# Kernel optimization log

Measured on AMD Instinct MI355X. Metric: run time of the kernel, lower is better.

Reference implementation:

```python
import jax, jax.numpy as jnp
import numpy as np

N, T, D, H1, H2, NH = 4096, 2048, 256, 128, 32, 4
ALPHA = 0.2  # LeakyReLU slope in GAT
NEG = -9e15  # mask value for non-edges


def _gat(x, adj, W, a_src, a_dst, fc_W, fc_b):
    # Multi-head GAT (pygat style), heads stacked on leading axis, then Linear fc.
    Wh = jnp.einsum('nd,hde->hne', x, W)                    # [NH, n, d_out]
    f = jnp.einsum('hne,he->hn', Wh, a_src)                 # a^T [Wh_i || .]
    g = jnp.einsum('hne,he->hn', Wh, a_dst)                 # a^T [. || Wh_j]
    e = jax.nn.leaky_relu(f[:, :, None] + g[:, None, :], ALPHA)  # [NH, n, n]
    e = jnp.where(adj[None, :, :] > 0, e, NEG)
    att = jax.nn.softmax(e, axis=-1)
    h = jax.nn.elu(jnp.einsum('hnm,hme->hne', att, Wh))     # concat=True -> ELU
    h = jnp.transpose(h, (1, 0, 2)).reshape(x.shape[0], -1)  # [n, NH*d_out]
    return h @ fc_W + fc_b


def setup_inputs() -> dict:
    key = jax.random.key(0)
    ks = jax.random.split(key, 24)
    s = 0.1
    x = jax.random.normal(ks[0], (N, D), jnp.float32)
    t_x = jax.random.normal(ks[1], (T, D), jnp.float32)
    adj = (jax.random.uniform(ks[2], (N, N)) < 0.005).astype(jnp.float32) + jnp.eye(N, dtype=jnp.float32)
    t_adj = (jax.random.uniform(ks[3], (T, T)) < 0.01).astype(jnp.float32) + jnp.eye(T, dtype=jnp.float32)
    tfidf_x = jax.random.uniform(ks[4], (T, N), jnp.float32) * 0.01
    p = lambda k, shp: jax.random.normal(k, shp, jnp.float32) * s
    return {
        'x': x, 'adj': adj, 't_x': t_x, 't_adj': t_adj, 'tfidf_x': tfidf_x,
        # concept-graph MHGAT (in D -> per-head D, concat NH*D -> fc -> D)
        'gat_W': p(ks[5], (NH, D, D)), 'gat_asrc': p(ks[6], (NH, D)), 'gat_adst': p(ks[7], (NH, D)),
        'gat_fcW': p(ks[8], (NH * D, D)), 'gat_fcb': jnp.zeros((D,), jnp.float32),
        # text-graph MHGAT
        't_W': p(ks[9], (NH, D, D)), 't_asrc': p(ks[10], (NH, D)), 't_adst': p(ks[11], (NH, D)),
        't_fcW': p(ks[12], (NH * D, D)), 't_fcb': jnp.zeros((D,), jnp.float32),
        # gated fusion fc
        'fus_W': p(ks[13], (D, D)), 'fus_b': jnp.zeros((D,), jnp.float32),
        # GCN encoder weights (Kipf VGAE GraphConvolution: adj @ (x @ W))
        'gc1_W': p(ks[14], (D, H1)), 'gc2_W': p(ks[15], (H1, H2)), 'gc3_W': p(ks[16], (H1, H2)),
    }


def reference(x, adj, t_x, t_adj, tfidf_x,
              gat_W, gat_asrc, gat_adst, gat_fcW, gat_fcb,
              t_W, t_asrc, t_adst, t_fcW, t_fcb,
              fus_W, fus_b, gc1_W, gc2_W, gc3_W):
    # gated fusion of concept-graph and text-graph GAT outputs (eval mode, dropout off)
    concept = _gat(x, adj, gat_W, gat_asrc, gat_adst, gat_fcW, gat_fcb)      # [N, D]
    gat_text = _gat(t_x, t_adj, t_W, t_asrc, t_adst, t_fcW, t_fcb)           # [T, D]
    c_text = tfidf_x.T @ gat_text                                            # [N, D]
    z = jax.nn.sigmoid(concept + c_text)
    fusion = (z * concept + (1.0 - z) * c_text) @ fus_W + fus_b              # [N, D]
    # GCN VAE encoder
    h1 = jax.nn.relu(adj @ (fusion @ gc1_W))                                 # [N, H1]
    mu = adj @ (h1 @ gc2_W)                                                  # [N, H2]
    logvar = adj @ (h1 @ gc3_W)                                              # [N, H2]
    # eval-mode reparameterize -> z_lat = mu; decoder act is identity in GCNModelVAE
    recon = mu @ mu.T                                                        # [N, N]
    return recon, mu, logvar
```

## Files before the change

kernel.cpp:

```cpp
#include <hip/hip_runtime.h>
#include <hip/hip_bf16.h>

#define MAX_E 128
typedef __attribute__((ext_vector_type(8))) short bf16x8;
typedef __attribute__((ext_vector_type(4))) float f32x4;

__device__ __forceinline__ unsigned short f2bf(float f) {
    union { float f; unsigned u; } a; a.f = f;
    unsigned r = a.u + 0x7FFFu + ((a.u >> 16) & 1u);
    return (unsigned short)(r >> 16);
}
__device__ __forceinline__ float bf2f(unsigned short s) {
    union { unsigned u; float f; } a; a.u = ((unsigned)s) << 16; return a.f;
}
__device__ __forceinline__ float wave_sum(float v) {
#pragma unroll
    for (int o = 1; o < 64; o <<= 1) v += __shfl_xor(v, o, 64);
    return v;
}
__device__ __forceinline__ float wave_max(float v) {
#pragma unroll
    for (int o = 1; o < 64; o <<= 1) v = fmaxf(v, __shfl_xor(v, o, 64));
    return v;
}

#define MAXJ 16
struct TJobs {
    const float* src[MAXJ];
    unsigned short* dst[MAXJ];
    int R[MAXJ], C[MAXJ], tb[MAXJ];
    int njobs;
};

__global__ __launch_bounds__(256) void prep_k(
        const float* __restrict__ adj, const float* __restrict__ t_adj,
        int* __restrict__ cnt, int* __restrict__ eidx_c, int* __restrict__ eidx_t,
        const float* __restrict__ gat_W, const float* __restrict__ gat_asrc,
        const float* __restrict__ gat_adst, const float* __restrict__ t_W,
        const float* __restrict__ t_asrc, const float* __restrict__ t_adst,
        float* __restrict__ APDP,
        const float* __restrict__ fus_W, const float* __restrict__ fus_b,
        const float* __restrict__ gc1_W, unsigned short* __restrict__ W2T,
        float* __restrict__ B2,
        const float* __restrict__ x, const float* __restrict__ t_x,
        unsigned short* __restrict__ XBF, unsigned short* __restrict__ TXBF,
        int w2_base, int cast_base, TJobs tj) {
    __shared__ float smem[2080];
    int bid = blockIdx.x, tid = threadIdx.x;
    if (bid < 6144) {
        int* s_cnt = (int*)smem;
        if (tid == 0) *s_cnt = 0;
        __syncthreads();
        if (bid < 4096) {
            const float4* ar = (const float4*)(adj + (size_t)bid * 4096);
            int* er = eidx_c + (size_t)bid * MAX_E;
            float4 v0 = ar[tid], v1 = ar[tid + 256], v2 = ar[tid + 512], v3 = ar[tid + 768];
            float va[16] = {v0.x, v0.y, v0.z, v0.w, v1.x, v1.y, v1.z, v1.w,
                            v2.x, v2.y, v2.z, v2.w, v3.x, v3.y, v3.z, v3.w};
#pragma unroll
            for (int it = 0; it < 4; it++) {
                int jb = (tid + it * 256) * 4;
#pragma unroll
                for (int c = 0; c < 4; c++) {
                    float vv = va[it * 4 + c];
                    if (vv > 0.f) {
                        int p = atomicAdd(s_cnt, 1);
                        if (p < MAX_E) er[p] = (jb + c) | (vv > 1.5f ? 0x40000000 : 0);
                    }
                }
            }
        } else {
            int r = bid - 4096;
            const float4* ar = (const float4*)(t_adj + (size_t)r * 2048);
            int* er = eidx_t + (size_t)r * MAX_E;
            float4 v0 = ar[tid], v1 = ar[tid + 256];
            float va[8] = {v0.x, v0.y, v0.z, v0.w, v1.x, v1.y, v1.z, v1.w};
#pragma unroll
            for (int it = 0; it < 2; it++) {
                int jb = (tid + it * 256) * 4;
#pragma unroll
                for (int c = 0; c < 4; c++) {
                    if (va[it * 4 + c] > 0.f) {
                        int p = atomicAdd(s_cnt, 1);
                        if (p < MAX_E) er[p] = jb + c;
                    }
                }
            }
        }
        __syncthreads();
        if (tid == 0) cnt[bid] = *s_cnt < MAX_E ? *s_cnt : MAX_E;
    } else if (bid < 6152) {
        int pb = bid - 6144, h = pb & 3, g = pb >> 2, d = tid;
        const float* W  = g ? t_W : gat_W;
        const float* as = g ? t_asrc : gat_asrc;
        const float* ad = g ? t_adst : gat_adst;
        float* sa = smem; float* sd = smem + 256;
        sa[d] = as[h * 256 + d]; sd[d] = ad[h * 256 + d];
        __syncthreads();
        const float* wr = W + (size_t)h * 65536 + (size_t)d * 256;
        float ap = 0.f, dp = 0.f;
        for (int e = 0; e < 256; e++) { float w = wr[e]; ap += w * sa[e]; dp += w * sd[e]; }
        APDP[g * 1024 + h * 256 + d] = ap;
        APDP[2048 + g * 1024 + h * 256 + d] = dp;
    } else if (bid < w2_base) {
        int local = bid - 6152;
        int j = 0;
        while (j + 1 < tj.njobs && local >= tj.tb[j + 1]) j++;
        local -= tj.tb[j];
        int R = tj.R[j], C = tj.C[j];
        int xt = C >> 5;
        int tx = local % xt, ty = local / xt;
        const float* in = tj.src[j];
        unsigned short* outp = tj.dst[j];
        float (*t)[33] = (float(*)[33])smem;
        int jj = tid & 31, ii = tid >> 5;
        int r0 = ty * 32, c0 = tx * 32;
#pragma unroll
        for (int k = 0; k < 4; k++) { int rl = ii + k * 8; t[rl][jj] = in[(size_t)(r0 + rl) * C + c0 + jj]; }
        __syncthreads();
#pragma unroll
        for (int k = 0; k < 4; k++) { int cl = ii + k * 8; outp[(size_t)(c0 + cl) * R + r0 + jj] = f2bf(t[jj][cl]); }
    } else if (bid < w2_base + 32) {
        int bW = bid - w2_base;
        int n0 = (bW & 3) * 32, k0 = (bW >> 2) * 32;
        int nn = tid & 31, kb = (tid >> 5) * 4;
        float (*s_a)[65] = (float(*)[65])smem;
        float acc[4] = {0.f, 0.f, 0.f, 0.f};
        for (int ec = 0; ec < 4; ec++) {
            for (int t = tid; t < 32 * 64; t += 256) {
                int kk2 = t >> 6, ee = t & 63;
                s_a[kk2][ee] = fus_W[(size_t)(k0 + kk2) * 256 + ec * 64 + ee];
            }
            __syncthreads();
            for (int ee = 0; ee < 64; ee++) {
                float b = gc1_W[(size_t)(ec * 64 + ee) * 128 + n0 + nn];
#pragma unroll
                for (int c = 0; c < 4; c++) acc[c] += s_a[kb + c][ee] * b;
            }
            __syncthreads();
        }
#pragma unroll
        for (int c = 0; c < 4; c++)
            W2T[(size_t)(n0 + nn) * 256 + k0 + kb + c] = f2bf(acc[c]);
    } else if (bid < cast_base) {
        if (tid < 128) {
            float acc = 0.f;
            for (int k = 0; k < 256; k++) acc += fus_b[k] * gc1_W[(size_t)k * 128 + tid];
            B2[tid] = acc;
        }
    } else {
        int local = bid - cast_base;
        const float4* src; unsigned short* dst; int li;
        if (local < 1024) { src = (const float4*)x; dst = XBF; li = local * 256 + tid; }
        else { src = (const float4*)t_x; dst = TXBF; li = (local - 1024) * 256 + tid; }
        float4 v = src[li];
        ushort4 o = {f2bf(v.x), f2bf(v.y), f2bf(v.z), f2bf(v.w)};
        *(ushort4*)(dst + (size_t)li * 4) = o;
    }
}

__device__ __forceinline__ void mfma_core(const unsigned short* __restrict__ A,
        const unsigned short* __restrict__ Bt, int K, int m0, int n0,
        unsigned short* As, unsigned short* Bs, f32x4 acc[4]) {
    int tid = threadIdx.x;
    int wave = tid >> 6, lane = tid & 63, quad = lane >> 4, r = lane & 15;
    int lrow = tid >> 2, lcol8 = (tid & 3) * 8;
    for (int k0 = 0; k0 < K; k0 += 32) {
        uint4 av = *(const uint4*)(A + (size_t)(m0 + lrow) * K + k0 + lcol8);
        uint4 bv = *(const uint4*)(Bt + (size_t)(n0 + lrow) * K + k0 + lcol8);
        *(uint4*)(&As[lrow * 40 + lcol8]) = av;
        *(uint4*)(&Bs[lrow * 40 + lcol8]) = bv;
        __syncthreads();
        bf16x8 af = *(const bf16x8*)(&As[(wave * 16 + r) * 40 + quad * 8]);
#pragma unroll
        for (int nj = 0; nj < 4; nj++) {
            bf16x8 bfr = *(const bf16x8*)(&Bs[(nj * 16 + r) * 40 + quad * 8]);
            acc[nj] = __builtin_amdgcn_mfma_f32_16x16x32_bf16(af, bfr, acc[nj], 0, 0, 0);
        }
        __syncthreads();
    }
}

__global__ __launch_bounds__(256) void whfg_k(
        const float* __restrict__ x, const float* __restrict__ t_x,
        const unsigned short* __restrict__ XBF, const unsigned short* __restrict__ TXBF,
        const unsigned short* __restrict__ WT, const unsigned short* __restrict__ TWT,
        unsigned short* __restrict__ WHC, unsigned short* __restrict__ WHT,
        const float* __restrict__ APDP, float* __restrict__ FC, float* __restrict__ GC,
        float* __restrict__ FT, float* __restrict__ GT) {
    __shared__ __align__(16) unsigned short As[64 * 40], Bs[64 * 40];
    int bid = blockIdx.x, tid = threadIdx.x;
    if (bid < 1536) {
        int g, xk, y, h;
        if (bid < 1024) { g = 0; xk = bid & 3; y = (bid >> 2) & 63; h = bid >> 8; }
        else { int b2 = bid - 1024; g = 1; xk = b2 & 3; y = (b2 >> 2) & 31; h = b2 >> 7; }
        const unsigned short* A = g ? TXBF : XBF;
        const unsigned short* Bt = (g ? TWT : WT) + h * 65536;
        unsigned short* C = (g ? WHT : WHC) + h * 256;
        int m0 = y * 64, n0 = xk * 64;
        f32x4 acc[4] = {{0.f,0.f,0.f,0.f},{0.f,0.f,0.f,0.f},{0.f,0.f,0.f,0.f},{0.f,0.f,0.f,0.f}};
        mfma_core(A, Bt, 256, m0, n0, As, Bs, acc);
        int wave = tid >> 6, lane = tid & 63, quad = lane >> 4, r = lane & 15;
#pragma unroll
        for (int nj = 0; nj < 4; nj++) {
            int n = n0 + nj * 16 + r;
#pragma unroll
            for (int reg = 0; reg < 4; reg++) {
                int m = m0 + wave * 16 + quad * 4 + reg;
                C[(size_t)m * 1024 + n] = f2bf(acc[nj][reg]);
            }
        }
    } else {
        int b = bid - 1536;
        int h = tid >> 6, lane = tid & 63;
        const float* xr; float* F; float* G; const float* AP; const float* DP; int n, i;
        if (b < 4096) { i = b; xr = x + (size_t)i * 256; F = FC; G = GC; AP = APDP; DP = APDP + 2048; n = 4096; }
        else { i = b - 4096; xr = t_x + (size_t)i * 256; F = FT; G = GT; AP = APDP + 1024; DP = APDP + 3072; n = 2048; }
        float vf = 0.f, vg = 0.f;
#pragma unroll
        for (int c = 0; c < 4; c++) {
            int d = c * 64 + lane;
            float xv = xr[d];
            vf += xv * AP[h * 256 + d];
            vg += xv * DP[h * 256 + d];
        }
        vf = wave_sum(vf); vg = wave_sum(vg);
        if (lane == 0) { F[h * n + i] = vf; G[h * n + i] = vg; }
    }
}

__global__ __launch_bounds__(256) void agg_all_k(const unsigned short* __restrict__ WHC,
        const unsigned short* __restrict__ WHT, const float* __restrict__ FC,
        const float* __restrict__ GC, const float* __restrict__ FT,
        const float* __restrict__ GT, const int* __restrict__ cnt,
        const int* __restrict__ eidx_c, const int* __restrict__ eidx_t,
        unsigned short* __restrict__ HCC, unsigned short* __restrict__ HCT) {
    int b = blockIdx.x, tid = threadIdx.x;
    int h = tid >> 6, lane = tid & 63;
    int ne = cnt[b];
    const unsigned short* WH; const float* F; const float* G; const int* ei;
    unsigned short* HC; int n, i;
    if (b < 4096) { i = b; n = 4096; WH = WHC; F = FC; G = GC; ei = eidx_c + (size_t)i * MAX_E; HC = HCC; }
    else { i = b - 4096; n = 2048; WH = WHT; F = FT; G = GT; ei = eidx_t + (size_t)i * MAX_E; HC = HCT; }
    __shared__ int s_col[MAX_E];
    __shared__ float s_w[4][MAX_E];
    for (int e = tid; e < ne; e += 256) s_col[e] = ei[e] & 0xFFFF;
    __syncthreads();
    float fi = F[h * n + i];
    float lmax = -1e30f;
    for (int e = lane; e < ne; e += 64) {
        float xv = fi + G[h * n + s_col[e]];
        xv = xv >= 0.f ? xv : 0.2f * xv;
        s_w[h][e] = xv;
        lmax = fmaxf(lmax, xv);
    }
    lmax = wave_max(lmax);
    float lsum = 0.f;
    for (int e = lane; e < ne; e += 64) {
        float w = __expf(s_w[h][e] - lmax);
        s_w[h][e] = w;
        lsum += w;
    }
    lsum = wave_sum(lsum);
    float inv = 1.f / lsum;
    float a0 = 0.f, a1 = 0.f, a2 = 0.f, a3 = 0.f;
    const unsigned short* base = WH + h * 256 + lane * 4;
    for (int e = 0; e < ne; e++) {
        float w = s_w[h][e];
        ushort4 q = *(const ushort4*)(base + (size_t)s_col[e] * 1024);
        a0 += w * bf2f(q.x); a1 += w * bf2f(q.y); a2 += w * bf2f(q.z); a3 += w * bf2f(q.w);
    }
    a0 *= inv; a1 *= inv; a2 *= inv; a3 *= inv;
    a0 = a0 > 0.f ? a0 : __expf(a0) - 1.f;
    a1 = a1 > 0.f ? a1 : __expf(a1) - 1.f;
    a2 = a2 > 0.f ? a2 : __expf(a2) - 1.f;
    a3 = a3 > 0.f ? a3 : __expf(a3) - 1.f;
    ushort4 st; st.x = f2bf(a0); st.y = f2bf(a1); st.z = f2bf(a2); st.w = f2bf(a3);
    *(ushort4*)(HC + (size_t)i * 1024 + h * 256 + lane * 4) = st;
}

__global__ __launch_bounds__(256) void fc_both_k(const unsigned short* __restrict__ HCC,
        const unsigned short* __restrict__ HCT, const unsigned short* __restrict__ FCWT,
        const unsigned short* __restrict__ TFCWT, const float* __restrict__ fcb,
        const float* __restrict__ tfcb, float* __restrict__ CPT,
        unsigned short* __restrict__ GTT) {
    __shared__ __align__(16) unsigned short As[64 * 40], Bs[64 * 40];
    int z = blockIdx.z;
    int M = z ? 2048 : 4096;
    int m0 = blockIdx.y * 64, n0 = blockIdx.x * 64;
    if (m0 >= M) return;
    const unsigned short* A = z ? HCT : HCC;
    const unsigned short* Bt = z ? TFCWT : FCWT;
    const float* bias = z ? tfcb : fcb;
    f32x4 acc[4] = {{0.f,0.f,0.f,0.f},{0.f,0.f,0.f,0.f},{0.f,0.f,0.f,0.f},{0.f,0.f,0.f,0.f}};
    mfma_core(A, Bt, 1024, m0, n0, As, Bs, acc);
    int tid = threadIdx.x, wave = tid >> 6, lane = tid & 63, quad = lane >> 4, r = lane & 15;
#pragma unroll
    for (int nj = 0; nj < 4; nj++) {
        int n = n0 + nj * 16 + r;
        float bv = bias[n];
        if (z == 0) {
#pragma unroll
            for (int reg = 0; reg < 4; reg++) {
                int m = m0 + wave * 16 + quad * 4 + reg;
                CPT[(size_t)m * 256 + n] = acc[nj][reg] + bv;
            }
        } else {
            int mb = m0 + wave * 16 + quad * 4;
            ushort4 st;
            st.x = f2bf(acc[nj][0] + bv); st.y = f2bf(acc[nj][1] + bv);
            st.z = f2bf(acc[nj][2] + bv); st.w = f2bf(acc[nj][3] + bv);
            *(ushort4*)(GTT + (size_t)n * 2048 + mb) = st;
        }
    }
}

__global__ __launch_bounds__(256) void ctext_splitk_k(
        const float* __restrict__ tfidf, const unsigned short* __restrict__ GTT,
        float* __restrict__ PART) {
    __shared__ float Asf[32 * 65];
    int tid = threadIdx.x;
    int wave = tid >> 6, lane = tid & 63, quad = lane >> 4, r = lane & 15;
    int kc = blockIdx.x;
    int m0 = blockIdx.y * 64;
    int kbase = kc * 256;
    int akk = tid >> 3, aseg = tid & 7;
    int mrel = wave * 16 + r;
    f32x4 acc[16];
#pragma unroll
    for (int i = 0; i < 16; i++) acc[i] = {0.f, 0.f, 0.f, 0.f};
    for (int k0 = 0; k0 < 256; k0 += 32) {
        const float* ap = tfidf + (size_t)(kbase + k0 + akk) * 4096 + m0 + aseg * 8;
        float4 a0 = *(const float4*)ap;
        float4 a1 = *(const float4*)(ap + 4);
        float av[8] = {a0.x, a0.y, a0.z, a0.w, a1.x, a1.y, a1.z, a1.w};
        __syncthreads();
#pragma unroll
        for (int i = 0; i < 8; i++) Asf[akk * 65 + aseg * 8 + i] = av[i];
        __syncthreads();
        bf16x8 af;
#pragma unroll
        for (int j = 0; j < 8; j++)
            af[j] = (short)f2bf(Asf[(quad * 8 + j) * 65 + mrel]);
#pragma unroll
        for (int nj = 0; nj < 16; nj++) {
            bf16x8 bfr = *(const bf16x8*)(GTT + (size_t)(nj * 16 + r) * 2048
                                          + kbase + k0 + quad * 8);
            acc[nj] = __builtin_amdgcn_mfma_f32_16x16x32_bf16(af, bfr, acc[nj], 0, 0, 0);
        }
    }
    float* P = PART + (size_t)kc * (4096 * 256);
#pragma unroll
    for (int nj = 0; nj < 16; nj++) {
        int n = nj * 16 + r;
#pragma unroll
        for (int reg = 0; reg < 4; reg++) {
            int m = m0 + wave * 16 + quad * 4 + reg;
            P[(size_t)m * 256 + n] = acc[nj][reg];
        }
    }
}

__global__ void gate_k(const float* __restrict__ PART, const float* __restrict__ CPT,
                       unsigned short* __restrict__ FUSEIN) {
    int idx = blockIdx.x * 256 + threadIdx.x;
    float4 s = ((const float4*)PART)[idx];
#pragma unroll
    for (int kc = 1; kc < 8; kc++) {
        float4 p = ((const float4*)PART)[(size_t)kc * 262144 + idx];
        s.x += p.x; s.y += p.y; s.z += p.z; s.w += p.w;
    }
    float4 c = ((const float4*)CPT)[idx];
    float cc[4] = {c.x, c.y, c.z, c.w}, ss[4] = {s.x, s.y, s.z, s.w};
    ushort4 st;
    unsigned short* o = (unsigned short*)&st;
#pragma unroll
    for (int i = 0; i < 4; i++) {
        float z = 1.f / (1.f + __expf(-(cc[i] + ss[i])));
        o[i] = f2bf(z * cc[i] + (1.f - z) * ss[i]);
    }
    *(ushort4*)(FUSEIN + (size_t)idx * 4) = st;
}

template <int EP>
__global__ __launch_bounds__(256) void gemm_ep_k(const unsigned short* __restrict__ A,
        const unsigned short* __restrict__ Bt, const float* __restrict__ bias,
        void* __restrict__ Cv, int M, int N, int K, int ldc) {
    __shared__ __align__(16) unsigned short As[64 * 40], Bs[64 * 40];
    int m0 = blockIdx.y * 64, n0 = blockIdx.x * 64;
    if (m0 >= M) return;
    f32x4 acc[4] = {{0.f,0.f,0.f,0.f},{0.f,0.f,0.f,0.f},{0.f,0.f,0.f,0.f},{0.f,0.f,0.f,0.f}};
    mfma_core(A, Bt, K, m0, n0, As, Bs, acc);
    int tid = threadIdx.x, wave = tid >> 6, lane = tid & 63, quad = lane >> 4, r = lane & 15;
#pragma unroll
    for (int nj = 0; nj < 4; nj++) {
        int n = n0 + nj * 16 + r;
        float bv = (EP == 1) ? bias[n] : 0.f;
#pragma unroll
        for (int reg = 0; reg < 4; reg++) {
            int m = m0 + wave * 16 + quad * 4 + reg;
            ((float*)Cv)[(size_t)m * ldc + n] = acc[nj][reg] + bv;
        }
    }
}

__global__ void spmm_h1_k(const int* __restrict__ cnt, const int* __restrict__ eidx,
                          const float* __restrict__ T1, unsigned short* __restrict__ H1B) {
    int i = blockIdx.x, tid = threadIdx.x;
    int ne = cnt[i];
    __shared__ int s_e[MAX_E];
    for (int e = tid; e < ne; e += 128) s_e[e] = eidx[(size_t)i * MAX_E + e];
    __syncthreads();
    float acc = 0.f;
    for (int e = 0; e < ne; e++) {
        int p = s_e[e];
        float v = (p & 0x40000000) ? 2.f : 1.f;
        acc += v * T1[(size_t)(p & 0xFFFF) * 128 + tid];
    }
    H1B[(size_t)i * 128 + tid] = f2bf(fmaxf(acc, 0.f));
}

__global__ void spmm_mu_k(const int* __restrict__ cnt, const int* __restrict__ eidx,
                          const unsigned short* __restrict__ H1B,
                          const unsigned short* __restrict__ GC23WT,
                          float* __restrict__ MU, float* __restrict__ LOGVAR,
                          unsigned short* __restrict__ MUBF) {
    int i = blockIdx.x, tid = threadIdx.x;
    int ne = cnt[i];
    __shared__ int s_e[MAX_E];
    __shared__ float s_a2[128];
    for (int e = tid; e < ne; e += 128) s_e[e] = eidx[(size_t)i * MAX_E + e];
    __syncthreads();
    float acc = 0.f;
    for (int e = 0; e < ne; e++) {
        int p = s_e[e];
        float v = (p & 0x40000000) ? 2.f : 1.f;
        acc += v * bf2f(H1B[(size_t)(p & 0xFFFF) * 128 + tid]);
    }
    s_a2[tid] = acc;
    __syncthreads();
    if (tid < 64) {
        const unsigned short* w = GC23WT + tid * 128;
        float o = 0.f;
        for (int k = 0; k < 128; k++) o += s_a2[k] * bf2f(w[k]);
        if (tid < 32) { MU[(size_t)i * 32 + tid] = o; MUBF[(size_t)i * 32 + tid] = f2bf(o); }
        else LOGVAR[(size_t)i * 32 + (tid - 32)] = o;
    }
}

extern "C" void kernel_launch(void* const* d_in, const int* in_sizes, int n_in,
                              void* d_out, int out_size, void* d_ws, size_t ws_size,
                              hipStream_t stream) {
    const float* x        = (const float*)d_in[0];
    const float* adj      = (const float*)d_in[1];
    const float* t_x      = (const float*)d_in[2];
    const float* t_adj    = (const float*)d_in[3];
    const float* tfidf    = (const float*)d_in[4];
    const float* gat_W    = (const float*)d_in[5];
    const float* gat_asrc = (const float*)d_in[6];
    const float* gat_adst = (const float*)d_in[7];
    const float* gat_fcW  = (const float*)d_in[8];
    const float* gat_fcb  = (const float*)d_in[9];
    const float* t_W      = (const float*)d_in[10];
    const float* t_asrc   = (const float*)d_in[11];
    const float* t_adst   = (const float*)d_in[12];
    const float* t_fcW    = (const float*)d_in[13];
    const float* t_fcb    = (const float*)d_in[14];
    const float* fus_W    = (const float*)d_in[15];
    const float* fus_b    = (const float*)d_in[16];
    const float* gc1_W    = (const float*)d_in[17];
    const float* gc2_W    = (const float*)d_in[18];
    const float* gc3_W    = (const float*)d_in[19];

    float* out = (float*)d_out;
    float* ws  = (float*)d_ws;

    unsigned short* WHC   = (unsigned short*)(ws + 0);
    unsigned short* HCC   = (unsigned short*)(ws + 2097152);
    unsigned short* WHT   = (unsigned short*)(ws + 4194304);
    unsigned short* HCT   = (unsigned short*)(ws + 5242880);
    float* PART           = ws + 0;
    float* CPT            = ws + 8388608;
    unsigned short* GTT   = (unsigned short*)(ws + 9437184);
    unsigned short* FUSEIN= (unsigned short*)(ws + 9699328);
    float* T1             = ws + 10223616;
    unsigned short* H1B   = (unsigned short*)(ws + 10747904);
    unsigned short* MUBF  = (unsigned short*)(ws + 11010048);
    float* FC             = ws + 11075584;
    float* GC             = ws + 11091968;
    float* FT             = ws + 11108352;
    float* GT             = ws + 11116544;
    float* APDP           = ws + 11124736;
    unsigned short* WT    = (unsigned short*)(ws + 11128832);
    unsigned short* TWT   = (unsigned short*)(ws + 11259904);
    unsigned short* FCWT  = (unsigned short*)(ws + 11390976);
    unsigned short* TFCWT = (unsigned short*)(ws + 11522048);
    unsigned short* W2T   = (unsigned short*)(ws + 11653120);
    float* B2             = ws + 11669504;
    unsigned short* GC23WT= (unsigned short*)(ws + 11669632);
    int* ECNT             = (int*)(ws + 11673728);
    int* EIDX_C           = (int*)(ws + 11679872);
    int* EIDX_T           = (int*)(ws + 12204160);
    unsigned short* XBF   = (unsigned short*)(ws + 12466304);
    unsigned short* TXBF  = (unsigned short*)(ws + 12990592);
    float* MU     = out + (size_t)4096 * 4096;
    float* LOGVAR = MU + (size_t)4096 * 32;

    TJobs tj = {};
    int nj = 0, tb = 0;
    auto add = [&](const float* s, unsigned short* d, int R, int C) {
        tj.src[nj] = s; tj.dst[nj] = d; tj.R[nj] = R; tj.C[nj] = C; tj.tb[nj] = tb;
        tb += (R >> 5) * (C >> 5); nj++;
    };
    for (int h = 0; h < 4; h++) add(gat_W + h * 65536, WT + h * 65536, 256, 256);
    for (int h = 0; h < 4; h++) add(t_W + h * 65536, TWT + h * 65536, 256, 256);
    add(gat_fcW, FCWT, 1024, 256);
    add(t_fcW, TFCWT, 1024, 256);
    add(gc2_W, GC23WT, 128, 32);
    add(gc3_W, GC23WT + 32 * 128, 128, 32);
    tj.njobs = nj;
    int w2_base = 6152 + tb;
    int cast_base = w2_base + 33;
    prep_k<<<cast_base + 1536, 256, 0, stream>>>(adj, t_adj, ECNT, EIDX_C, EIDX_T,
        gat_W, gat_asrc, gat_adst, t_W, t_asrc, t_adst, APDP,
        fus_W, fus_b, gc1_W, W2T, B2, x, t_x, XBF, TXBF, w2_base, cast_base, tj);

    whfg_k<<<1536 + 6144, 256, 0, stream>>>(x, t_x, XBF, TXBF, WT, TWT, WHC, WHT,
                                            APDP, FC, GC, FT, GT);

    agg_all_k<<<6144, 256, 0, stream>>>(WHC, WHT, FC, GC, FT, GT, ECNT, EIDX_C, EIDX_T, HCC, HCT);

    fc_both_k<<<dim3(4, 64, 2), 256, 0, stream>>>(HCC, HCT, FCWT, TFCWT, gat_fcb, t_fcb, CPT, GTT);

    ctext_splitk_k<<<dim3(8, 64), 256, 0, stream>>>(tfidf, GTT, PART);

    gate_k<<<1024, 256, 0, stream>>>(PART, CPT, FUSEIN);

    gemm_ep_k<1><<<dim3(2, 64), 256, 0, stream>>>(FUSEIN, W2T, B2, T1, 4096, 128, 256, 128);

    spmm_h1_k<<<4096, 128, 0, stream>>>(ECNT, EIDX_C, T1, H1B);

    spmm_mu_k<<<4096, 128, 0, stream>>>(ECNT, EIDX_C, H1B, GC23WT, MU, LOGVAR, MUBF);

    gemm_ep_k<0><<<dim3(64, 64), 256, 0, stream>>>(MUBF, MUBF, nullptr, out, 4096, 4096, 32, 4096);
}
```

Measured before the change: 346.8 us.

## Use wave-per-row ballot compaction for edges and stage ctext B tiles in LDS

Edge-list extraction now gives each adjacency row to one wavefront and compacts with ballot/popcount instead of a per-block shared atomic counter, cutting the block count fourfold. The x/t_x bf16 cast blocks each process four float4 chunks per thread. In ctext_splitk_k the GTT B fragments are loaded cooperatively into padded shared memory once per k-step, replacing repeated strided global loads by each wave. Edge ordering stays deterministic per row. The kernel uses more LDS, which may lower occupancy.

```diff
diff --git a/kernel.cpp b/kernel.cpp
--- a/kernel.cpp
+++ b/kernel.cpp
@@ -47,50 +47,60 @@
         int w2_base, int cast_base, TJobs tj) {
     __shared__ float smem[2080];
     int bid = blockIdx.x, tid = threadIdx.x;
-    if (bid < 6144) {
-        int* s_cnt = (int*)smem;
-        if (tid == 0) *s_cnt = 0;
-        __syncthreads();
-        if (bid < 4096) {
-            const float4* ar = (const float4*)(adj + (size_t)bid * 4096);
-            int* er = eidx_c + (size_t)bid * MAX_E;
-            float4 v0 = ar[tid], v1 = ar[tid + 256], v2 = ar[tid + 512], v3 = ar[tid + 768];
-            float va[16] = {v0.x, v0.y, v0.z, v0.w, v1.x, v1.y, v1.z, v1.w,
-                            v2.x, v2.y, v2.z, v2.w, v3.x, v3.y, v3.z, v3.w};
-#pragma unroll
-            for (int it = 0; it < 4; it++) {
-                int jb = (tid + it * 256) * 4;
+    if (bid < 1536) {
+        int wave = tid >> 6, lane = tid & 63;
+        unsigned long long lmask = (1ull << lane) - 1ull;
+        if (bid < 1024) {
+            int row = bid * 4 + wave;
+            const float4* ar = (const float4*)(adj + (size_t)row * 4096);
+            int* er = eidx_c + (size_t)row * MAX_E;
+            float4 v[16];
+#pragma unroll
+            for (int it = 0; it < 16; it++) v[it] = ar[it * 64 + lane];
+            int base = 0;
+#pragma unroll
+            for (int it = 0; it < 16; it++) {
+                int jb = (it * 64 + lane) * 4;
 #pragma unroll
                 for (int c = 0; c < 4; c++) {
-                    float vv = va[it * 4 + c];
-                    if (vv > 0.f) {
-                        int p = atomicAdd(s_cnt, 1);
-                        if (p < MAX_E) er[p] = (jb + c) | (vv > 1.5f ? 0x40000000 : 0);
+                    float vv = c == 0 ? v[it].x : c == 1 ? v[it].y : c == 2 ? v[it].z : v[it].w;
+                    bool nz = vv > 0.f;
+                    unsigned long long mask = __ballot(nz);
+                    if (nz) {
+                        int pos = base + __popcll(mask & lmask);
+                        if (pos < MAX_E) er[pos] = (jb + c) | (vv > 1.5f ? 0x40000000 : 0);
                     }
+                    base += __popcll(mask);
                 }
             }
+            if (lane == 0) cnt[row] = base < MAX_E ? base : MAX_E;
         } else {
-            int r = bid - 4096;
-            const float4* ar = (const float4*)(t_adj + (size_t)r * 2048);
-            int* er = eidx_t + (size_t)r * MAX_E;
-            float4 v0 = ar[tid], v1 = ar[tid + 256];
-            float va[8] = {v0.x, v0.y, v0.z, v0.w, v1.x, v1.y, v1.z, v1.w};
-#pragma unroll
-            for (int it = 0; it < 2; it++) {
-                int jb = (tid + it * 256) * 4;
+            int row = (bid - 1024) * 4 + wave;
+            const float4* ar = (const float4*)(t_adj + (size_t)row * 2048);
+            int* er = eidx_t + (size_t)row * MAX_E;
+            float4 v[8];
+#pragma unroll
+            for (int it = 0; it < 8; it++) v[it] = ar[it * 64 + lane];
+            int base = 0;
+#pragma unroll
+            for (int it = 0; it < 8; it++) {
+                int jb = (it * 64 + lane) * 4;
 #pragma unroll
                 for (int c = 0; c < 4; c++) {
-                    if (va[it * 4 + c] > 0.f) {
-                        int p = atomicAdd(s_cnt, 1);
-                        if (p < MAX_E) er[p] = jb + c;
+                    float vv = c == 0 ? v[it].x : c == 1 ? v[it].y : c == 2 ? v[it].z : v[it].w;
+                    bool nz = vv > 0.f;
+                    unsigned long long mask = __ballot(nz);
+                    if (nz) {
+                        int pos = base + __popcll(mask & lmask);
+                        if (pos < MAX_E) er[pos] = jb + c;
                     }
+                    base += __popcll(mask);
                 }
             }
-        }
-        __syncthreads();
-        if (tid == 0) cnt[bid] = *s_cnt < MAX_E ? *s_cnt : MAX_E;
-    } else if (bid < 6152) {
-        int pb = bid - 6144, h = pb & 3, g = pb >> 2, d = tid;
+            if (lane == 0) cnt[4096 + row] = base < MAX_E ? base : MAX_E;
+        }
+    } else if (bid < 1544) {
+        int pb = bid - 1536, h = pb & 3, g = pb >> 2, d = tid;
         const float* W  = g ? t_W : gat_W;
         const float* as = g ? t_asrc : gat_asrc;
         const float* ad = g ? t_adst : gat_adst;
@@ -103,7 +113,7 @@
         APDP[g * 1024 + h * 256 + d] = ap;
         APDP[2048 + g * 1024 + h * 256 + d] = dp;
     } else if (bid < w2_base) {
-        int local = bid - 6152;
+        int local = bid - 1544;
         int j = 0;
         while (j + 1 < tj.njobs && local >= tj.tb[j + 1]) j++;
         local -= tj.tb[j];
@@ -150,12 +160,16 @@
         }
     } else {
         int local = bid - cast_base;
-        const float4* src; unsigned short* dst; int li;
-        if (local < 1024) { src = (const float4*)x; dst = XBF; li = local * 256 + tid; }
-        else { src = (const float4*)t_x; dst = TXBF; li = (local - 1024) * 256 + tid; }
-        float4 v = src[li];
-        ushort4 o = {f2bf(v.x), f2bf(v.y), f2bf(v.z), f2bf(v.w)};
-        *(ushort4*)(dst + (size_t)li * 4) = o;
+        const float4* src; unsigned short* dst; int fbase;
+        if (local < 256) { src = (const float4*)x; dst = XBF; fbase = local * 1024; }
+        else { src = (const float4*)t_x; dst = TXBF; fbase = (local - 256) * 1024; }
+#pragma unroll
+        for (int k = 0; k < 4; k++) {
+            int li = fbase + k * 256 + tid;
+            float4 v = src[li];
+            ushort4 o = {f2bf(v.x), f2bf(v.y), f2bf(v.z), f2bf(v.w)};
+            *(ushort4*)(dst + (size_t)li * 4) = o;
+        }
     }
 }
 
@@ -319,6 +333,7 @@
         const float* __restrict__ tfidf, const unsigned short* __restrict__ GTT,
         float* __restrict__ PART) {
     __shared__ float Asf[32 * 65];
+    __shared__ __align__(16) unsigned short Bs[256 * 40];
     int tid = threadIdx.x;
     int wave = tid >> 6, lane = tid & 63, quad = lane >> 4, r = lane & 15;
     int kc = blockIdx.x;
@@ -333,10 +348,16 @@
         const float* ap = tfidf + (size_t)(kbase + k0 + akk) * 4096 + m0 + aseg * 8;
         float4 a0 = *(const float4*)ap;
         float4 a1 = *(const float4*)(ap + 4);
+        const uint4* bsrc = (const uint4*)(GTT + (size_t)tid * 2048 + kbase + k0);
+        uint4 b0 = bsrc[0], b1 = bsrc[1], b2 = bsrc[2], b3 = bsrc[3];
         float av[8] = {a0.x, a0.y, a0.z, a0.w, a1.x, a1.y, a1.z, a1.w};
         __syncthreads();
 #pragma unroll
         for (int i = 0; i < 8; i++) Asf[akk * 65 + aseg * 8 + i] = av[i];
+        {
+            uint4* bd = (uint4*)(&Bs[tid * 40]);
+            bd[0] = b0; bd[1] = b1; bd[2] = b2; bd[3] = b3;
+        }
         __syncthreads();
         bf16x8 af;
 #pragma unroll
@@ -344,8 +365,7 @@
             af[j] = (short)f2bf(Asf[(quad * 8 + j) * 65 + mrel]);
 #pragma unroll
         for (int nj = 0; nj < 16; nj++) {
-            bf16x8 bfr = *(const bf16x8*)(GTT + (size_t)(nj * 16 + r) * 2048
-                                          + kbase + k0 + quad * 8);
+            bf16x8 bfr = *(const bf16x8*)(&Bs[(nj * 16 + r) * 40 + quad * 8]);
             acc[nj] = __builtin_amdgcn_mfma_f32_16x16x32_bf16(af, bfr, acc[nj], 0, 0, 0);
         }
     }
@@ -519,9 +539,9 @@
     add(gc2_W, GC23WT, 128, 32);
     add(gc3_W, GC23WT + 32 * 128, 128, 32);
     tj.njobs = nj;
-    int w2_base = 6152 + tb;
+    int w2_base = 1544 + tb;
     int cast_base = w2_base + 33;
-    prep_k<<<cast_base + 1536, 256, 0, stream>>>(adj, t_adj, ECNT, EIDX_C, EIDX_T,
+    prep_k<<<cast_base + 384, 256, 0, stream>>>(adj, t_adj, ECNT, EIDX_C, EIDX_T,
         gat_W, gat_asrc, gat_adst, t_W, t_asrc, t_adst, APDP,
         fus_W, fus_b, gc1_W, W2T, B2, x, t_x, XBF, TXBF, w2_base, cast_base, tj);
 
```

After: 327.7 us. 5.5% less time.
